# Kernel tuning notes

Measured on AMD Instinct MI355X. Metric: run time of the kernel, lower is better.

## Reference

```python
import jax, jax.numpy as jnp
import numpy as np

N_NODES = 100000
N_EDGES = 500000
N_REL = 3
IN_F, HID_F, OUT_F = 128, 128, 128
H_HALF = OUT_F // 2  # BiLSTM hidden per direction


def setup_inputs() -> dict:
    key = jax.random.key(0)
    ks = jax.random.split(key, 16)
    s = 0.05
    inp = {
        "x": jax.random.normal(ks[0], (N_NODES, IN_F), jnp.float32),
        "src": jax.random.randint(ks[1], (N_REL, N_EDGES), 0, N_NODES),
        "dst": jax.random.randint(ks[2], (N_REL, N_EDGES), 0, N_NODES),
        # per-relation GraphConv weights (layer 1 and 2)
        "W1": jax.random.normal(ks[3], (N_REL, IN_F, HID_F), jnp.float32) * s,
        "b1": jnp.zeros((N_REL, HID_F), jnp.float32),
        "W2": jax.random.normal(ks[4], (N_REL, HID_F, OUT_F), jnp.float32) * s,
        "b2": jnp.zeros((N_REL, OUT_F), jnp.float32),
        # BiLSTM (1 layer, seq_len=1); PyTorch gate order i,f,g,o
        "Wih_f": jax.random.normal(ks[5], (4 * H_HALF, OUT_F), jnp.float32) * s,
        "Whh_f": jax.random.normal(ks[6], (4 * H_HALF, H_HALF), jnp.float32) * s,
        "bih_f": jnp.zeros((4 * H_HALF,), jnp.float32),
        "bhh_f": jnp.zeros((4 * H_HALF,), jnp.float32),
        "Wih_b": jax.random.normal(ks[7], (4 * H_HALF, OUT_F), jnp.float32) * s,
        "Whh_b": jax.random.normal(ks[8], (4 * H_HALF, H_HALF), jnp.float32) * s,
        "bih_b": jnp.zeros((4 * H_HALF,), jnp.float32),
        "bhh_b": jnp.zeros((4 * H_HALF,), jnp.float32),
    }
    return inp


def _hetero_conv(x, src, dst, W, b):
    """HeteroGraphConv(GraphConv, norm='both'), mean-aggregated over relations.
    x: [N,Din]; src,dst: [R,E]; W: [R,Din,Dout]; b: [R,Dout] -> [N,Dout]."""
    n = x.shape[0]

    def rel_conv(s, d, w, bb):
        ones = jnp.ones(s.shape[0], x.dtype)
        deg_out = jnp.clip(jax.ops.segment_sum(ones, s, num_segments=n), 1.0)
        deg_in = jnp.clip(jax.ops.segment_sum(ones, d, num_segments=n), 1.0)
        # weight first (in_feats >= out_feats path in DGL); math-equivalent
        xw = (x * jax.lax.rsqrt(deg_out)[:, None]) @ w          # [N,Dout]
        agg = jax.ops.segment_sum(xw[s], d, num_segments=n)     # [N,Dout]
        return agg * jax.lax.rsqrt(deg_in)[:, None] + bb

    outs = jax.vmap(rel_conv)(src, dst, W, b)  # [R,N,Dout]
    return jnp.mean(outs, axis=0)


def _lstm_step(x, Wih, bih, bhh):
    # single LSTM step from zero (h0, c0); Whh contributes nothing
    g = x @ Wih.T + bih + bhh
    i, f, gg, o = jnp.split(g, 4, axis=-1)
    c = jax.nn.sigmoid(i) * jnp.tanh(gg)
    return jax.nn.sigmoid(o) * jnp.tanh(c)


def reference(x, src, dst, W1, b1, W2, b2,
              Wih_f, Whh_f, bih_f, bhh_f,
              Wih_b, Whh_b, bih_b, bhh_b):
    h = jax.nn.relu(_hetero_conv(x, src, dst, W1, b1))
    h = _hetero_conv(h, src, dst, W2, b2)          # [N, OUT_F]
    hf = _lstm_step(h, Wih_f, bih_f, bhh_f)        # [N, H_HALF]
    hb = _lstm_step(h, Wih_b, bih_b, bhh_b)        # [N, H_HALF]
    return jnp.concatenate([hf, hb], axis=-1)      # [N, OUT_F]
```

## Files before the change

kernel.cpp:

```cpp
#include <hip/hip_runtime.h>
#include <hip/hip_fp16.h>
#include <math.h>

#define NN 100000
#define NE 500000
#define NREL 3
#define F 128
#define SCAN_BLK 1024
#define NBLK ((NN + SCAN_BLK - 1) / SCAN_BLK)
#define CH 25000
#define NCH 4

#define RANGE 16384
#define NRANGE 7
#define NPAD (NRANGE * RANGE)
#define EC 20
#define EPC (NE / EC)

typedef __attribute__((ext_vector_type(8))) short bf16x8;
typedef __attribute__((ext_vector_type(4))) float f32x4;

__device__ __forceinline__ float sigm(float x) { return 1.f / (1.f + __expf(-x)); }

__device__ __forceinline__ unsigned bf16rne(float x) {
  unsigned u = __float_as_uint(x);
  return (u + 0x7FFFu + ((u >> 16) & 1u)) >> 16;
}
__device__ __forceinline__ void split1(float x, unsigned& h, unsigned& l) {
  h = bf16rne(x);
  float hf = __uint_as_float(h << 16);
  l = bf16rne(x - hf);
}

__global__ __launch_bounds__(256) void hist_part(const int* __restrict__ src,
                                                 const int* __restrict__ dst,
                                                 int* __restrict__ part) {
  int x = blockIdx.x & 7, q = blockIdx.x >> 3;
  int g = q % NRANGE;
  int rc2 = x + 8 * (q / NRANGE);
  int a = rc2 / (NREL * EC);
  int rcl = rc2 % (NREL * EC);
  int r = rcl / EC, c = rcl % EC;
  __shared__ int h[RANGE];
  for (int i = threadIdx.x; i < RANGE; i += 256) h[i] = 0;
  __syncthreads();
  const int* idx = (a ? dst : src) + (size_t)r * NE + (size_t)c * EPC;
  const int4* v4 = (const int4*)idx;
  int lo = g * RANGE;
  for (int i = threadIdx.x; i < EPC / 4; i += 256) {
    int4 v = v4[i];
    int t;
    t = v.x - lo; if ((unsigned)t < RANGE) atomicAdd(&h[t], 1);
    t = v.y - lo; if ((unsigned)t < RANGE) atomicAdd(&h[t], 1);
    t = v.z - lo; if ((unsigned)t < RANGE) atomicAdd(&h[t], 1);
    t = v.w - lo; if ((unsigned)t < RANGE) atomicAdd(&h[t], 1);
  }
  __syncthreads();
  int* op = part + (((size_t)a * NREL + r) * EC + c) * NPAD + (size_t)g * RANGE;
  for (int i = threadIdx.x; i < RANGE; i += 256) op[i] = h[i];
}

__global__ void reduce_part(const int* __restrict__ part, int* __restrict__ cnt_out,
                            int* __restrict__ cnt_in) {
  int i = blockIdx.x * blockDim.x + threadIdx.x;
  if (i >= 2 * NREL * NN) return;
  int a = i / (NREL * NN);
  int rn = i - a * (NREL * NN);
  const int* p = part + ((size_t)a * NREL + rn / NN) * EC * NPAD + (rn % NN);
  int s = 0;
#pragma unroll
  for (int c = 0; c < EC; ++c) s += p[(size_t)c * NPAD];
  (a ? cnt_in : cnt_out)[rn] = s;
}

__global__ void make_rs(const int* __restrict__ cnt_out, const int* __restrict__ cnt_in,
                        float* __restrict__ rs_out, float* __restrict__ rs_in3) {
  int i = blockIdx.x * blockDim.x + threadIdx.x;
  if (i >= NREL * NN) return;
  int c0 = cnt_out[i];
  rs_out[i] = rsqrtf((float)(c0 < 1 ? 1 : c0));
  int c1 = cnt_in[i];
  rs_in3[i] = rsqrtf((float)(c1 < 1 ? 1 : c1)) * (1.f / 3.f);
}

__global__ __launch_bounds__(256) void scan1(const int* __restrict__ cnt,
                                             int* __restrict__ excl, int* __restrict__ bsums) {
  int rb = blockIdx.x;
  int r = rb / NBLK, blk = rb % NBLK;
  int tid = (int)threadIdx.x;
  int v[4]; int sum = 0;
#pragma unroll
  for (int i = 0; i < 4; ++i) {
    int idx = blk * SCAN_BLK + tid * 4 + i;
    int c = (idx < NN) ? cnt[r * NN + idx] : 0;
    v[i] = sum; sum += c;
  }
  __shared__ int ts[256];
  ts[tid] = sum;
  __syncthreads();
  for (int off = 1; off < 256; off <<= 1) {
    int t = (tid >= off) ? ts[tid - off] : 0;
    __syncthreads();
    ts[tid] += t;
    __syncthreads();
  }
  int texcl = tid ? ts[tid - 1] : 0;
#pragma unroll
  for (int i = 0; i < 4; ++i) {
    int idx = blk * SCAN_BLK + tid * 4 + i;
    if (idx < NN) excl[r * NN + idx] = texcl + v[i];
  }
  if (tid == 255) bsums[rb] = ts[255];
}

__global__ __launch_bounds__(128) void scan2(int* __restrict__ bsums) {
  int r = blockIdx.x;
  int tid = (int)threadIdx.x;
  __shared__ int ts[128];
  ts[tid] = (tid < NBLK) ? bsums[r * NBLK + tid] : 0;
  __syncthreads();
  for (int off = 1; off < 128; off <<= 1) {
    int t = (tid >= off) ? ts[tid - off] : 0;
    __syncthreads();
    ts[tid] += t;
    __syncthreads();
  }
  if (tid < NBLK) bsums[r * NBLK + tid] = tid ? ts[tid - 1] : 0;
}

__global__ void scan3(int* __restrict__ row_ptr, const int* __restrict__ bsums) {
  int i = blockIdx.x * blockDim.x + threadIdx.x;
  if (i >= NREL * NN) return;
  int r = i / NN, idx = i - r * NN, blk = idx / SCAN_BLK;
  row_ptr[i] += bsums[r * NBLK + blk];
}

__global__ void chunk_prefix(int* __restrict__ part_dst, const int* __restrict__ row_ptr) {
  int i = blockIdx.x * blockDim.x + threadIdx.x;
  if (i >= NREL * NN) return;
  int r = i / NN, node = i - r * NN;
  int* p = part_dst + (size_t)r * EC * NPAD + node;
  int run = row_ptr[i];
#pragma unroll
  for (int c = 0; c < EC; ++c) {
    int t = p[(size_t)c * NPAD];
    p[(size_t)c * NPAD] = run;
    run += t;
  }
}

__global__ void make_pay(const int* __restrict__ src, const float* __restrict__ rs_out,
                         int2* __restrict__ pay) {
  int i = blockIdx.x * blockDim.x + threadIdx.x;
  if (i >= NREL * NE) return;
  int r = i / NE;
  int s = src[i];
  pay[i] = make_int2(s, __float_as_int(rs_out[r * NN + s]));
}

__global__ __launch_bounds__(256) void place_part(const int* __restrict__ dst,
                                                  const int2* __restrict__ pay,
                                                  const int* __restrict__ part_dst,
                                                  int2* __restrict__ ses) {
  int x = blockIdx.x & 7, q = blockIdx.x >> 3;
  int g = q % NRANGE;
  int rc = x + 8 * (q / NRANGE);
  if (rc >= NREL * EC) return;
  int r = rc / EC, c = rc % EC;
  __shared__ int cur[RANGE];
  const int* pc = part_dst + ((size_t)r * EC + c) * NPAD + (size_t)g * RANGE;
  for (int i = threadIdx.x; i < RANGE; i += 256) cur[i] = pc[i];
  __syncthreads();
  int lo = g * RANGE;
  const int4* d4 = (const int4*)(dst + (size_t)r * NE + (size_t)c * EPC);
  const int4* p4 = (const int4*)(pay + (size_t)r * NE + (size_t)c * EPC);
  int2* sesr = ses + (size_t)r * NE;
  for (int i = threadIdx.x; i < EPC / 4; i += 256) {
    int4 dv = d4[i];
    int4 pa = p4[2 * i], pb = p4[2 * i + 1];
    int t;
    t = dv.x - lo; if ((unsigned)t < RANGE) { int pos = atomicAdd(&cur[t], 1); sesr[pos] = make_int2(pa.x, pa.y); }
    t = dv.y - lo; if ((unsigned)t < RANGE) { int pos = atomicAdd(&cur[t], 1); sesr[pos] = make_int2(pa.z, pa.w); }
    t = dv.z - lo; if ((unsigned)t < RANGE) { int pos = atomicAdd(&cur[t], 1); sesr[pos] = make_int2(pb.x, pb.y); }
    t = dv.w - lo; if ((unsigned)t < RANGE) { int pos = atomicAdd(&cur[t], 1); sesr[pos] = make_int2(pb.z, pb.w); }
  }
}

__global__ void prep_small(const float* __restrict__ b1, const float* __restrict__ b2,
                           const float* __restrict__ bif, const float* __restrict__ bhf,
                           const float* __restrict__ bib, const float* __restrict__ bhb,
                           float* __restrict__ bbar1, float* __restrict__ bbar2,
                           float* __restrict__ bselw) {
  int t = (int)threadIdx.x;
  if (t < 128) {
    bbar1[t] = (b1[t] + b1[128 + t] + b1[256 + t]) * (1.f / 3.f);
  } else if (t < 256) {
    int j = t - 128;
    bbar2[j] = (b2[j] + b2[128 + j] + b2[256 + j]) * (1.f / 3.f);
  } else if (t < 640) {
    int m = t - 256;
    int g = m >> 7, j = m & 127, dir = j >> 6, jj = j & 63;
    int grow = (g == 0) ? jj : (g == 1) ? (128 + jj) : (192 + jj);
    bselw[m] = dir ? (bib[grow] + bhb[grow]) : (bif[grow] + bhf[grow]);
  }
}

__global__ void wt_split(const float* __restrict__ W, ushort* __restrict__ th,
                         ushort* __restrict__ tl) {
  int i = blockIdx.x * blockDim.x + threadIdx.x;
  if (i >= 128 * 384) return;
  int n = i / 384, k = i % 384;
  float v = W[(size_t)k * 128 + n];
  unsigned h, l; split1(v, h, l);
  th[i] = (ushort)h; tl[i] = (ushort)l;
}

__global__ void pack_w_split(const float* __restrict__ Wf, const float* __restrict__ Wb,
                             ushort* __restrict__ ph, ushort* __restrict__ pl) {
  int i = blockIdx.x * blockDim.x + threadIdx.x;
  if (i >= 384 * 128) return;
  int m = i / 128, k = i % 128;
  int g = m >> 7, j = m & 127, dir = j >> 6, jj = j & 63;
  int grow = (g == 0) ? jj : (g == 1) ? (128 + jj) : (192 + jj);
  float v = (dir ? Wb : Wf)[(size_t)grow * 128 + k];
  unsigned h, l; split1(v, h, l);
  ph[i] = (ushort)h; pl[i] = (ushort)l;
}

__global__ void cvt_f16(const float* __restrict__ in, ushort* __restrict__ o16) {
  int i = blockIdx.x * blockDim.x + threadIdx.x;
  if (i >= NN * (F / 4)) return;
  float4 v = ((const float4*)in)[i];
  __half2 a = __floats2half2_rn(v.x, v.y);
  __half2 b = __floats2half2_rn(v.z, v.w);
  ((uint2*)o16)[i] = make_uint2(*(unsigned*)&a, *(unsigned*)&b);
}

__global__ __launch_bounds__(256) void gather3(
    const ushort* __restrict__ table, const int2* __restrict__ ses,
    const int* __restrict__ row_ptr, const int* __restrict__ cnt,
    const float* __restrict__ rs_in3, ushort* __restrict__ z_h,
    ushort* __restrict__ z_l, int n0) {
  int wid = (int)threadIdx.x >> 6, lane = (int)threadIdx.x & 63;
  int gw = blockIdx.x * 4 + wid;
  int r = gw / CH;
  int n = n0 + (gw - r * CH);
  int base = r * NN + n;
  int beg = row_ptr[base], c = cnt[base];
  const int2* el = ses + (size_t)r * NE + beg;
  int half = lane >> 5, cl = lane & 31;
  const uint2* x2 = (const uint2*)table + cl;
  float4 acc = make_float4(0.f, 0.f, 0.f, 0.f);

  int p = 0;
  while (p < c) {
    int rem = c - p; if (rem > 16) rem = 16;
    int2 es = make_int2(0, 0);
    if (lane < rem) es = el[p + lane];
    uint2 rw[8]; float scv[8];
#pragma unroll
    for (int j = 0; j < 8; ++j) {
      int e = 2 * j + half;
      int idx = (e < rem) ? e : 0;
      int s = __shfl(es.x, idx);
      float sc = __int_as_float(__shfl(es.y, idx));
      if (e >= rem) sc = 0.f;
      if (2 * j < rem) {
        rw[j] = x2[(size_t)s * 32];
        scv[j] = sc;
      }
    }
#pragma unroll
    for (int j = 0; j < 8; ++j) {
      if (2 * j < rem) {
        float2 f0 = __half22float2(*(__half2*)&rw[j].x);
        float2 f1 = __half22float2(*(__half2*)&rw[j].y);
        float sc = scv[j];
        acc.x = fmaf(f0.x, sc, acc.x); acc.y = fmaf(f0.y, sc, acc.y);
        acc.z = fmaf(f1.x, sc, acc.z); acc.w = fmaf(f1.y, sc, acc.w);
      }
    }
    p += rem;
  }

  acc.x += __shfl_xor(acc.x, 32);
  acc.y += __shfl_xor(acc.y, 32);
  acc.z += __shfl_xor(acc.z, 32);
  acc.w += __shfl_xor(acc.w, 32);
  float ci = rs_in3[base];
  unsigned h[4], l[4];
  split1(acc.x * ci, h[0], l[0]); split1(acc.y * ci, h[1], l[1]);
  split1(acc.z * ci, h[2], l[2]); split1(acc.w * ci, h[3], l[3]);
  size_t zo = (size_t)(n - n0) * 384 + r * 128 + cl * 4;
  if (half == 0) {
    *(ushort2*)(z_h + zo) = make_ushort2((ushort)h[0], (ushort)h[1]);
    *(ushort2*)(z_h + zo + 2) = make_ushort2((ushort)h[2], (ushort)h[3]);
  } else {
    *(ushort2*)(z_l + zo) = make_ushort2((ushort)l[0], (ushort)l[1]);
    *(ushort2*)(z_l + zo + 2) = make_ushort2((ushort)l[2], (ushort)l[3]);
  }
}

__device__ __forceinline__ int swz(int row, int slot) {
  return row * 32 + ((slot ^ ((row >> 1) & 3)) << 3);
}

template <bool RELU, bool OUT16>
__global__ __launch_bounds__(256) void gemm_mfma(
    const ushort* __restrict__ zh, const ushort* __restrict__ zl,
    const ushort* __restrict__ wth, const ushort* __restrict__ wtl,
    const float* __restrict__ bias, void* __restrict__ Hout, int n0) {
  __shared__ ushort Ash[64 * 32], Asl[64 * 32], Bsh[128 * 32], Bsl[128 * 32];
  const int row0 = blockIdx.x * 64;
  const int t = (int)threadIdx.x;
  const int wn = t >> 6, l = t & 63, lr = l & 15, lk = l >> 4;
  f32x4 acc[4][2];
#pragma unroll
  for (int a = 0; a < 4; ++a)
#pragma unroll
    for (int b = 0; b < 2; ++b) acc[a][b] = (f32x4){0.f, 0.f, 0.f, 0.f};

  for (int kt = 0; kt < 12; ++kt) {
    __syncthreads();
    {
      int rr = t >> 2, slot = t & 3;
      size_t go = (size_t)(row0 + rr) * 384 + kt * 32 + slot * 8;
      uint4 vh = make_uint4(0, 0, 0, 0), vl = make_uint4(0, 0, 0, 0);
      if (row0 + rr < CH) { vh = *(const uint4*)(zh + go); vl = *(const uint4*)(zl + go); }
      *(uint4*)&Ash[swz(rr, slot)] = vh;
      *(uint4*)&Asl[swz(rr, slot)] = vl;
    }
#pragma unroll
    for (int i = 0; i < 2; ++i) {
      int s = i * 256 + t;
      int nn_ = s >> 2, slot = s & 3;
      size_t go = (size_t)nn_ * 384 + kt * 32 + slot * 8;
      *(uint4*)&Bsh[swz(nn_, slot)] = *(const uint4*)(wth + go);
      *(uint4*)&Bsl[swz(nn_, slot)] = *(const uint4*)(wtl + go);
    }
    __syncthreads();
    bf16x8 ah[4], al[4], bh[2], bl[2];
#pragma unroll
    for (int mf = 0; mf < 4; ++mf) {
      int row = mf * 16 + lr;
      int off = swz(row, lk);
      ah[mf] = *(const bf16x8*)&Ash[off];
      al[mf] = *(const bf16x8*)&Asl[off];
    }
#pragma unroll
    for (int f = 0; f < 2; ++f) {
      int col = wn * 32 + f * 16 + lr;
      int off = swz(col, lk);
      bh[f] = *(const bf16x8*)&Bsh[off];
      bl[f] = *(const bf16x8*)&Bsl[off];
    }
#pragma unroll
    for (int mf = 0; mf < 4; ++mf)
#pragma unroll
      for (int f = 0; f < 2; ++f) {
        acc[mf][f] = __builtin_amdgcn_mfma_f32_16x16x32_bf16(ah[mf], bh[f], acc[mf][f], 0, 0, 0);
        acc[mf][f] = __builtin_amdgcn_mfma_f32_16x16x32_bf16(ah[mf], bl[f], acc[mf][f], 0, 0, 0);
        acc[mf][f] = __builtin_amdgcn_mfma_f32_16x16x32_bf16(al[mf], bh[f], acc[mf][f], 0, 0, 0);
      }
  }
#pragma unroll
  for (int mf = 0; mf < 4; ++mf)
#pragma unroll
    for (int f = 0; f < 2; ++f) {
      int col = wn * 32 + f * 16 + lr;
      float bv = bias[col];
#pragma unroll
      for (int reg = 0; reg < 4; ++reg) {
        int row = row0 + mf * 16 + lk * 4 + reg;
        if (row < CH) {
          float v = acc[mf][f][reg] + bv;
          if (RELU) v = fmaxf(v, 0.f);
          if (OUT16) {
            __half hv = __float2half_rn(v);
            ((ushort*)Hout)[(size_t)(n0 + row) * 128 + col] = *(ushort*)&hv;
          } else {
            ((float*)Hout)[(size_t)(n0 + row) * 128 + col] = v;
          }
        }
      }
    }
}

__global__ __launch_bounds__(512) void lstm_mfma(
    const float* __restrict__ H, const ushort* __restrict__ wph,
    const ushort* __restrict__ wpl, const float* __restrict__ bselw,
    float* __restrict__ out) {
  __shared__ ushort Ash[128 * 32], Asl[128 * 32], Bsh[384 * 32], Bsl[384 * 32];
  const int row0 = blockIdx.x * 128;
  const int t = (int)threadIdx.x;
  const int wid = t >> 6, wm = wid >> 2, wn = wid & 3;
  const int l = t & 63, lr = l & 15, lk = l >> 4;

  int j0 = wn * 16 + lr, j1 = (wn + 4) * 16 + lr;
  float bi0 = bselw[j0], bg0 = bselw[128 + j0], bo0 = bselw[256 + j0];
  float bi1 = bselw[j1], bg1 = bselw[128 + j1], bo1 = bselw[256 + j1];

  f32x4 acc[4][6];
#pragma unroll
  for (int a = 0; a < 4; ++a)
#pragma unroll
    for (int b = 0; b < 6; ++b) acc[a][b] = (f32x4){0.f, 0.f, 0.f, 0.f};

  for (int kt = 0; kt < 4; ++kt) {
    __syncthreads();
    {
      int rr = t >> 2, slot = t & 3;
      int grow = row0 + rr;
      float v[8];
      if (grow < NN) {
        float4 a0 = *(const float4*)(H + (size_t)grow * 128 + kt * 32 + slot * 8);
        float4 a1 = *(const float4*)(H + (size_t)grow * 128 + kt * 32 + slot * 8 + 4);
        v[0] = a0.x; v[1] = a0.y; v[2] = a0.z; v[3] = a0.w;
        v[4] = a1.x; v[5] = a1.y; v[6] = a1.z; v[7] = a1.w;
      } else {
#pragma unroll
        for (int q = 0; q < 8; ++q) v[q] = 0.f;
      }
      unsigned h[8], lo[8];
#pragma unroll
      for (int q = 0; q < 8; ++q) split1(v[q], h[q], lo[q]);
      uint4 hv = make_uint4(h[0] | (h[1] << 16), h[2] | (h[3] << 16),
                            h[4] | (h[5] << 16), h[6] | (h[7] << 16));
      uint4 lv = make_uint4(lo[0] | (lo[1] << 16), lo[2] | (lo[3] << 16),
                            lo[4] | (lo[5] << 16), lo[6] | (lo[7] << 16));
      *(uint4*)&Ash[swz(rr, slot)] = hv;
      *(uint4*)&Asl[swz(rr, slot)] = lv;
    }
#pragma unroll
    for (int i = 0; i < 3; ++i) {
      int s = i * 512 + t;
      int nn_ = s >> 2, slot = s & 3;
      size_t go = (size_t)nn_ * 128 + kt * 32 + slot * 8;
      *(uint4*)&Bsh[swz(nn_, slot)] = *(const uint4*)(wph + go);
      *(uint4*)&Bsl[swz(nn_, slot)] = *(const uint4*)(wpl + go);
    }
    __syncthreads();
    bf16x8 ah[4], al[4];
#pragma unroll
    for (int mf = 0; mf < 4; ++mf) {
      int row = wm * 64 + mf * 16 + lr;
      int off = swz(row, lk);
      ah[mf] = *(const bf16x8*)&Ash[off];
      al[mf] = *(const bf16x8*)&Asl[off];
    }
#pragma unroll
    for (int tt = 0; tt < 6; ++tt) {
      int col = (wn + 4 * tt) * 16 + lr;
      int off = swz(col, lk);
      bf16x8 bh = *(const bf16x8*)&Bsh[off];
      bf16x8 bl = *(const bf16x8*)&Bsl[off];
#pragma unroll
      for (int mf = 0; mf < 4; ++mf) {
        acc[mf][tt] = __builtin_amdgcn_mfma_f32_16x16x32_bf16(ah[mf], bh, acc[mf][tt], 0, 0, 0);
        acc[mf][tt] = __builtin_amdgcn_mfma_f32_16x16x32_bf16(ah[mf], bl, acc[mf][tt], 0, 0, 0);
        acc[mf][tt] = __builtin_amdgcn_mfma_f32_16x16x32_bf16(al[mf], bh, acc[mf][tt], 0, 0, 0);
      }
    }
  }
#pragma unroll
  for (int mf = 0; mf < 4; ++mf)
#pragma unroll
    for (int reg = 0; reg < 4; ++reg) {
      int row = row0 + wm * 64 + mf * 16 + lk * 4 + reg;
      if (row < NN) {
        float iv0 = acc[mf][0][reg] + bi0, gv0 = acc[mf][2][reg] + bg0, ov0 = acc[mf][4][reg] + bo0;
        float cc0 = sigm(iv0) * tanhf(gv0);
        out[(size_t)row * 128 + j0] = sigm(ov0) * tanhf(cc0);
        float iv1 = acc[mf][1][reg] + bi1, gv1 = acc[mf][3][reg] + bg1, ov1 = acc[mf][5][reg] + bo1;
        float cc1 = sigm(iv1) * tanhf(gv1);
        out[(size_t)row * 128 + j1] = sigm(ov1) * tanhf(cc1);
      }
    }
}

extern "C" void kernel_launch(void* const* d_in, const int* in_sizes, int n_in,
                              void* d_out, int out_size, void* d_ws, size_t ws_size,
                              hipStream_t stream) {
  const float* x = (const float*)d_in[0];
  const int* src = (const int*)d_in[1];
  const int* dst = (const int*)d_in[2];
  const float* W1 = (const float*)d_in[3];
  const float* b1 = (const float*)d_in[4];
  const float* W2 = (const float*)d_in[5];
  const float* b2 = (const float*)d_in[6];
  const float* Wih_f = (const float*)d_in[7];
  const float* bih_f = (const float*)d_in[9];
  const float* bhh_f = (const float*)d_in[10];
  const float* Wih_b = (const float*)d_in[11];
  const float* bih_b = (const float*)d_in[13];
  const float* bhh_b = (const float*)d_in[14];
  float* out = (float*)d_out;

  char* wp = (char*)d_ws;
  float* rs_out = (float*)wp;          wp += (size_t)3 * NN * 4;
  float* rs_in3 = (float*)wp;          wp += (size_t)3 * NN * 4;
  int* cnt_out = (int*)wp;             wp += (size_t)3 * NN * 4;
  int* cnt_in = (int*)wp;              wp += (size_t)3 * NN * 4;
  int* row_ptr = (int*)wp;             wp += (size_t)3 * NN * 4;
  int* bsums = (int*)wp;               wp += 4096;
  int2* ses = (int2*)wp;               wp += (size_t)3 * NE * 8;
  ushort* wt1h = (ushort*)wp;          wp += (size_t)128 * 384 * 2;
  ushort* wt1l = (ushort*)wp;          wp += (size_t)128 * 384 * 2;
  ushort* wt2h = (ushort*)wp;          wp += (size_t)128 * 384 * 2;
  ushort* wt2l = (ushort*)wp;          wp += (size_t)128 * 384 * 2;
  ushort* wph = (ushort*)wp;           wp += (size_t)384 * 128 * 2;
  ushort* wpl = (ushort*)wp;           wp += (size_t)384 * 128 * 2;
  float* bbar1 = (float*)wp;           wp += 512;
  float* bbar2 = (float*)wp;           wp += 512;
  float* bselw = (float*)wp;           wp += 2048;
  ushort* z_h = (ushort*)wp;           wp += (size_t)CH * 384 * 2;
  ushort* z_l = (ushort*)wp;           wp += (size_t)CH * 384 * 2;
  ushort* x16 = (ushort*)wp;           wp += (size_t)NN * F * 2;
  ushort* h116 = (ushort*)wp;          wp += (size_t)NN * F * 2;

  int* part = (int*)z_h;
  int* part_dst = part + (size_t)NREL * EC * NPAD;
  int2* pay = (int2*)h116;

  hist_part<<<8 * ((2 * NREL * EC + 7) / 8) * NRANGE, 256, 0, stream>>>(src, dst, part);
  reduce_part<<<(2 * NREL * NN + 255) / 256, 256, 0, stream>>>(part, cnt_out, cnt_in);
  make_rs<<<(NREL * NN + 255) / 256, 256, 0, stream>>>(cnt_out, cnt_in, rs_out, rs_in3);
  scan1<<<NREL * NBLK, 256, 0, stream>>>(cnt_in, row_ptr, bsums);
  scan2<<<NREL, 128, 0, stream>>>(bsums);
  scan3<<<(NREL * NN + 255) / 256, 256, 0, stream>>>(row_ptr, bsums);
  chunk_prefix<<<(NREL * NN + 255) / 256, 256, 0, stream>>>(part_dst, row_ptr);
  make_pay<<<(NREL * NE + 255) / 256, 256, 0, stream>>>(src, rs_out, pay);
  place_part<<<8 * ((NREL * EC + 7) / 8) * NRANGE, 256, 0, stream>>>(dst, pay, part_dst, ses);

  prep_small<<<1, 640, 0, stream>>>(b1, b2, bih_f, bhh_f, bih_b, bhh_b, bbar1, bbar2, bselw);
  wt_split<<<192, 256, 0, stream>>>(W1, wt1h, wt1l);
  wt_split<<<192, 256, 0, stream>>>(W2, wt2h, wt2l);
  pack_w_split<<<192, 256, 0, stream>>>(Wih_f, Wih_b, wph, wpl);
  cvt_f16<<<(NN * 32 + 255) / 256, 256, 0, stream>>>(x, x16);

  for (int c = 0; c < NCH; ++c) {
    gather3<<<3 * CH / 4, 256, 0, stream>>>(x16, ses, row_ptr, cnt_in, rs_in3, z_h, z_l, c * CH);
    gemm_mfma<true, true><<<(CH + 63) / 64, 256, 0, stream>>>(z_h, z_l, wt1h, wt1l, bbar1, h116, c * CH);
  }
  for (int c = 0; c < NCH; ++c) {
    gather3<<<3 * CH / 4, 256, 0, stream>>>(h116, ses, row_ptr, cnt_in, rs_in3, z_h, z_l, c * CH);
    gemm_mfma<false, false><<<(CH + 63) / 64, 256, 0, stream>>>(z_h, z_l, wt2h, wt2l, bbar2, out, c * CH);
  }
  lstm_mfma<<<(NN + 127) / 128, 512, 0, stream>>>(out, wph, wpl, bselw, out);
}
```

Measured before the change: 570.3 us.

## Store gathered activations as fp16 and fuse layer-2 GEMM with LSTM

The gather kernel now writes one fp16 intermediate instead of separate bf16 hi/lo planes, and the GEMM kernels split it into hi/lo bf16 when staging into shared memory. The layer-2 GraphConv GEMM is fused with the LSTM projection, so the layer-2 output stays in LDS and is never written to and re-read from global memory as fp32. This cuts intermediate memory traffic and one kernel launch. In exchange it adds fp16 rounding of the aggregated features and uses a larger LDS footprint and 512-thread blocks, which may lower occupancy.

```diff
diff --git a/kernel.cpp b/kernel.cpp
--- a/kernel.cpp
+++ b/kernel.cpp
@@ -30,6 +30,10 @@
   h = bf16rne(x);
   float hf = __uint_as_float(h << 16);
   l = bf16rne(x - hf);
+}
+
+__device__ __forceinline__ int swz(int row, int slot) {
+  return row * 32 + ((slot ^ ((row >> 1) & 3)) << 3);
 }
 
 __global__ __launch_bounds__(256) void hist_part(const int* __restrict__ src,
@@ -239,8 +243,7 @@
 __global__ __launch_bounds__(256) void gather3(
     const ushort* __restrict__ table, const int2* __restrict__ ses,
     const int* __restrict__ row_ptr, const int* __restrict__ cnt,
-    const float* __restrict__ rs_in3, ushort* __restrict__ z_h,
-    ushort* __restrict__ z_l, int n0) {
+    const float* __restrict__ rs_in3, ushort* __restrict__ z16, int n0) {
   int wid = (int)threadIdx.x >> 6, lane = (int)threadIdx.x & 63;
   int gw = blockIdx.x * 4 + wid;
   int r = gw / CH;
@@ -287,29 +290,34 @@
   acc.y += __shfl_xor(acc.y, 32);
   acc.z += __shfl_xor(acc.z, 32);
   acc.w += __shfl_xor(acc.w, 32);
-  float ci = rs_in3[base];
-  unsigned h[4], l[4];
-  split1(acc.x * ci, h[0], l[0]); split1(acc.y * ci, h[1], l[1]);
-  split1(acc.z * ci, h[2], l[2]); split1(acc.w * ci, h[3], l[3]);
-  size_t zo = (size_t)(n - n0) * 384 + r * 128 + cl * 4;
   if (half == 0) {
-    *(ushort2*)(z_h + zo) = make_ushort2((ushort)h[0], (ushort)h[1]);
-    *(ushort2*)(z_h + zo + 2) = make_ushort2((ushort)h[2], (ushort)h[3]);
-  } else {
-    *(ushort2*)(z_l + zo) = make_ushort2((ushort)l[0], (ushort)l[1]);
-    *(ushort2*)(z_l + zo + 2) = make_ushort2((ushort)l[2], (ushort)l[3]);
-  }
-}
-
-__device__ __forceinline__ int swz(int row, int slot) {
-  return row * 32 + ((slot ^ ((row >> 1) & 3)) << 3);
-}
-
-template <bool RELU, bool OUT16>
-__global__ __launch_bounds__(256) void gemm_mfma(
-    const ushort* __restrict__ zh, const ushort* __restrict__ zl,
+    float ci = rs_in3[base];
+    __half2 p0 = __floats2half2_rn(acc.x * ci, acc.y * ci);
+    __half2 p1 = __floats2half2_rn(acc.z * ci, acc.w * ci);
+    size_t zo = (size_t)(n - n0) * 384 + r * 128 + cl * 4;
+    *(uint2*)(z16 + zo) = make_uint2(*(unsigned*)&p0, *(unsigned*)&p1);
+  }
+}
+
+__device__ __forceinline__ void cvt_split8(uint4 v, uint4& hv, uint4& lv) {
+  float f[8];
+  *(float2*)&f[0] = __half22float2(*(__half2*)&v.x);
+  *(float2*)&f[2] = __half22float2(*(__half2*)&v.y);
+  *(float2*)&f[4] = __half22float2(*(__half2*)&v.z);
+  *(float2*)&f[6] = __half22float2(*(__half2*)&v.w);
+  unsigned h[8], l[8];
+#pragma unroll
+  for (int q = 0; q < 8; ++q) split1(f[q], h[q], l[q]);
+  hv = make_uint4(h[0] | (h[1] << 16), h[2] | (h[3] << 16),
+                  h[4] | (h[5] << 16), h[6] | (h[7] << 16));
+  lv = make_uint4(l[0] | (l[1] << 16), l[2] | (l[3] << 16),
+                  l[4] | (l[5] << 16), l[6] | (l[7] << 16));
+}
+
+__global__ __launch_bounds__(256) void gemm_mfma1(
+    const ushort* __restrict__ z16,
     const ushort* __restrict__ wth, const ushort* __restrict__ wtl,
-    const float* __restrict__ bias, void* __restrict__ Hout, int n0) {
+    const float* __restrict__ bias, ushort* __restrict__ Hout, int n0) {
   __shared__ ushort Ash[64 * 32], Asl[64 * 32], Bsh[128 * 32], Bsl[128 * 32];
   const int row0 = blockIdx.x * 64;
   const int t = (int)threadIdx.x;
@@ -324,11 +332,12 @@
     __syncthreads();
     {
       int rr = t >> 2, slot = t & 3;
-      size_t go = (size_t)(row0 + rr) * 384 + kt * 32 + slot * 8;
-      uint4 vh = make_uint4(0, 0, 0, 0), vl = make_uint4(0, 0, 0, 0);
-      if (row0 + rr < CH) { vh = *(const uint4*)(zh + go); vl = *(const uint4*)(zl + go); }
-      *(uint4*)&Ash[swz(rr, slot)] = vh;
-      *(uint4*)&Asl[swz(rr, slot)] = vl;
+      uint4 v = make_uint4(0, 0, 0, 0);
+      if (row0 + rr < CH)
+        v = *(const uint4*)(z16 + (size_t)(row0 + rr) * 384 + kt * 32 + slot * 8);
+      uint4 hv, lv; cvt_split8(v, hv, lv);
+      *(uint4*)&Ash[swz(rr, slot)] = hv;
+      *(uint4*)&Asl[swz(rr, slot)] = lv;
     }
 #pragma unroll
     for (int i = 0; i < 2; ++i) {
@@ -342,15 +351,13 @@
     bf16x8 ah[4], al[4], bh[2], bl[2];
 #pragma unroll
     for (int mf = 0; mf < 4; ++mf) {
-      int row = mf * 16 + lr;
-      int off = swz(row, lk);
+      int off = swz(mf * 16 + lr, lk);
       ah[mf] = *(const bf16x8*)&Ash[off];
       al[mf] = *(const bf16x8*)&Asl[off];
     }
 #pragma unroll
     for (int f = 0; f < 2; ++f) {
-      int col = wn * 32 + f * 16 + lr;
-      int off = swz(col, lk);
+      int off = swz(wn * 32 + f * 16 + lr, lk);
       bh[f] = *(const bf16x8*)&Bsh[off];
       bl[f] = *(const bf16x8*)&Bsl[off];
     }
@@ -373,107 +380,154 @@
       for (int reg = 0; reg < 4; ++reg) {
         int row = row0 + mf * 16 + lk * 4 + reg;
         if (row < CH) {
-          float v = acc[mf][f][reg] + bv;
-          if (RELU) v = fmaxf(v, 0.f);
-          if (OUT16) {
-            __half hv = __float2half_rn(v);
-            ((ushort*)Hout)[(size_t)(n0 + row) * 128 + col] = *(ushort*)&hv;
-          } else {
-            ((float*)Hout)[(size_t)(n0 + row) * 128 + col] = v;
-          }
+          float v = fmaxf(acc[mf][f][reg] + bv, 0.f);
+          __half hv = __float2half_rn(v);
+          Hout[(size_t)(n0 + row) * 128 + col] = *(ushort*)&hv;
         }
       }
     }
 }
 
-__global__ __launch_bounds__(512) void lstm_mfma(
-    const float* __restrict__ H, const ushort* __restrict__ wph,
-    const ushort* __restrict__ wpl, const float* __restrict__ bselw,
-    float* __restrict__ out) {
-  __shared__ ushort Ash[128 * 32], Asl[128 * 32], Bsh[384 * 32], Bsl[384 * 32];
-  const int row0 = blockIdx.x * 128;
+__global__ __launch_bounds__(512) void gemm2_lstm(
+    const ushort* __restrict__ z16,
+    const ushort* __restrict__ wth, const ushort* __restrict__ wtl,
+    const ushort* __restrict__ wph, const ushort* __restrict__ wpl,
+    const float* __restrict__ bbar2, const float* __restrict__ bselw,
+    float* __restrict__ out, int n0) {
+  __shared__ ushort lds[40960];
+  ushort* A1h = lds;
+  ushort* A1l = lds + 2048;
+  ushort* B1h = lds + 4096;
+  ushort* B1l = lds + 8192;
+  ushort* A2h = lds;
+  ushort* A2l = lds + 8192;
+  ushort* B3h = lds + 16384;
+  ushort* B3l = lds + 28672;
+
+  const int row0 = blockIdx.x * 64;
   const int t = (int)threadIdx.x;
-  const int wid = t >> 6, wm = wid >> 2, wn = wid & 3;
-  const int l = t & 63, lr = l & 15, lk = l >> 4;
-
-  int j0 = wn * 16 + lr, j1 = (wn + 4) * 16 + lr;
+  const int wid = t >> 6, l = t & 63, lr = l & 15, lk = l >> 4;
+
+  f32x4 acc1[4];
+#pragma unroll
+  for (int a = 0; a < 4; ++a) acc1[a] = (f32x4){0.f, 0.f, 0.f, 0.f};
+
+  for (int kt = 0; kt < 12; ++kt) {
+    __syncthreads();
+    if (t < 256) {
+      int rr = t >> 2, slot = t & 3;
+      uint4 v = make_uint4(0, 0, 0, 0);
+      if (row0 + rr < CH)
+        v = *(const uint4*)(z16 + (size_t)(row0 + rr) * 384 + kt * 32 + slot * 8);
+      uint4 hv, lv; cvt_split8(v, hv, lv);
+      *(uint4*)&A1h[swz(rr, slot)] = hv;
+      *(uint4*)&A1l[swz(rr, slot)] = lv;
+    }
+    {
+      int nn_ = t >> 2, slot = t & 3;
+      size_t go = (size_t)nn_ * 384 + kt * 32 + slot * 8;
+      *(uint4*)&B1h[swz(nn_, slot)] = *(const uint4*)(wth + go);
+      *(uint4*)&B1l[swz(nn_, slot)] = *(const uint4*)(wtl + go);
+    }
+    __syncthreads();
+    bf16x8 ah[4], al[4];
+#pragma unroll
+    for (int mf = 0; mf < 4; ++mf) {
+      int off = swz(mf * 16 + lr, lk);
+      ah[mf] = *(const bf16x8*)&A1h[off];
+      al[mf] = *(const bf16x8*)&A1l[off];
+    }
+    int offb = swz(wid * 16 + lr, lk);
+    bf16x8 bh = *(const bf16x8*)&B1h[offb];
+    bf16x8 bl = *(const bf16x8*)&B1l[offb];
+#pragma unroll
+    for (int mf = 0; mf < 4; ++mf) {
+      acc1[mf] = __builtin_amdgcn_mfma_f32_16x16x32_bf16(ah[mf], bh, acc1[mf], 0, 0, 0);
+      acc1[mf] = __builtin_amdgcn_mfma_f32_16x16x32_bf16(ah[mf], bl, acc1[mf], 0, 0, 0);
+      acc1[mf] = __builtin_amdgcn_mfma_f32_16x16x32_bf16(al[mf], bh, acc1[mf], 0, 0, 0);
+    }
+  }
+
+  __syncthreads();
+  {
+    int colc = wid * 16 + lr;
+    float bb = bbar2[colc];
+#pragma unroll
+    for (int mf = 0; mf < 4; ++mf)
+#pragma unroll
+      for (int reg = 0; reg < 4; ++reg) {
+        int rowc = mf * 16 + lk * 4 + reg;
+        float v = acc1[mf][reg] + bb;
+        unsigned h, lo2; split1(v, h, lo2);
+        int sl2 = (colc >> 3) ^ (rowc & 7);
+        int addr = rowc * 128 + (sl2 << 3) + (colc & 7);
+        A2h[addr] = (ushort)h;
+        A2l[addr] = (ushort)lo2;
+      }
+  }
+  __syncthreads();
+
+  const int wm = wid >> 2, wn3 = wid & 3;
+  f32x4 acc3[2][6];
+#pragma unroll
+  for (int a = 0; a < 2; ++a)
+#pragma unroll
+    for (int b = 0; b < 6; ++b) acc3[a][b] = (f32x4){0.f, 0.f, 0.f, 0.f};
+
+  for (int kt = 0; kt < 4; ++kt) {
+    if (kt) __syncthreads();
+#pragma unroll
+    for (int i = 0; i < 3; ++i) {
+      int s = i * 512 + t;
+      int m = s >> 2, slot = s & 3;
+      size_t go = (size_t)m * 128 + kt * 32 + slot * 8;
+      *(uint4*)&B3h[swz(m, slot)] = *(const uint4*)(wph + go);
+      *(uint4*)&B3l[swz(m, slot)] = *(const uint4*)(wpl + go);
+    }
+    __syncthreads();
+    bf16x8 ah2[2], al2[2];
+#pragma unroll
+    for (int mf = 0; mf < 2; ++mf) {
+      int row = wm * 32 + mf * 16 + lr;
+      int kslot = kt * 4 + lk;
+      int sl2 = kslot ^ (row & 7);
+      int addr = row * 128 + (sl2 << 3);
+      ah2[mf] = *(const bf16x8*)&A2h[addr];
+      al2[mf] = *(const bf16x8*)&A2l[addr];
+    }
+#pragma unroll
+    for (int tt = 0; tt < 6; ++tt) {
+      int m = (wn3 + 4 * tt) * 16 + lr;
+      int off = swz(m, lk);
+      bf16x8 bh = *(const bf16x8*)&B3h[off];
+      bf16x8 bl = *(const bf16x8*)&B3l[off];
+#pragma unroll
+      for (int mf = 0; mf < 2; ++mf) {
+        acc3[mf][tt] = __builtin_amdgcn_mfma_f32_16x16x32_bf16(ah2[mf], bh, acc3[mf][tt], 0, 0, 0);
+        acc3[mf][tt] = __builtin_amdgcn_mfma_f32_16x16x32_bf16(ah2[mf], bl, acc3[mf][tt], 0, 0, 0);
+        acc3[mf][tt] = __builtin_amdgcn_mfma_f32_16x16x32_bf16(al2[mf], bh, acc3[mf][tt], 0, 0, 0);
+      }
+    }
+  }
+
+  int j0 = wn3 * 16 + lr, j1 = j0 + 64;
   float bi0 = bselw[j0], bg0 = bselw[128 + j0], bo0 = bselw[256 + j0];
   float bi1 = bselw[j1], bg1 = bselw[128 + j1], bo1 = bselw[256 + j1];
-
-  f32x4 acc[4][6];
-#pragma unroll
-  for (int a = 0; a < 4; ++a)
-#pragma unroll
-    for (int b = 0; b < 6; ++b) acc[a][b] = (f32x4){0.f, 0.f, 0.f, 0.f};
-
-  for (int kt = 0; kt < 4; ++kt) {
-    __syncthreads();
-    {
-      int rr = t >> 2, slot = t & 3;
-      int grow = row0 + rr;
-      float v[8];
-      if (grow < NN) {
-        float4 a0 = *(const float4*)(H + (size_t)grow * 128 + kt * 32 + slot * 8);
-        float4 a1 = *(const float4*)(H + (size_t)grow * 128 + kt * 32 + slot * 8 + 4);
-        v[0] = a0.x; v[1] = a0.y; v[2] = a0.z; v[3] = a0.w;
-        v[4] = a1.x; v[5] = a1.y; v[6] = a1.z; v[7] = a1.w;
-      } else {
-#pragma unroll
-        for (int q = 0; q < 8; ++q) v[q] = 0.f;
-      }
-      unsigned h[8], lo[8];
-#pragma unroll
-      for (int q = 0; q < 8; ++q) split1(v[q], h[q], lo[q]);
-      uint4 hv = make_uint4(h[0] | (h[1] << 16), h[2] | (h[3] << 16),
-                            h[4] | (h[5] << 16), h[6] | (h[7] << 16));
-      uint4 lv = make_uint4(lo[0] | (lo[1] << 16), lo[2] | (lo[3] << 16),
-                            lo[4] | (lo[5] << 16), lo[6] | (lo[7] << 16));
-      *(uint4*)&Ash[swz(rr, slot)] = hv;
-      *(uint4*)&Asl[swz(rr, slot)] = lv;
-    }
-#pragma unroll
-    for (int i = 0; i < 3; ++i) {
-      int s = i * 512 + t;
-      int nn_ = s >> 2, slot = s & 3;
-      size_t go = (size_t)nn_ * 128 + kt * 32 + slot * 8;
-      *(uint4*)&Bsh[swz(nn_, slot)] = *(const uint4*)(wph + go);
-      *(uint4*)&Bsl[swz(nn_, slot)] = *(const uint4*)(wpl + go);
-    }
-    __syncthreads();
-    bf16x8 ah[4], al[4];
-#pragma unroll
-    for (int mf = 0; mf < 4; ++mf) {
-      int row = wm * 64 + mf * 16 + lr;
-      int off = swz(row, lk);
-      ah[mf] = *(const bf16x8*)&Ash[off];
-      al[mf] = *(const bf16x8*)&Asl[off];
-    }
-#pragma unroll
-    for (int tt = 0; tt < 6; ++tt) {
-      int col = (wn + 4 * tt) * 16 + lr;
-      int off = swz(col, lk);
-      bf16x8 bh = *(const bf16x8*)&Bsh[off];
-      bf16x8 bl = *(const bf16x8*)&Bsl[off];
-#pragma unroll
-      for (int mf = 0; mf < 4; ++mf) {
-        acc[mf][tt] = __builtin_amdgcn_mfma_f32_16x16x32_bf16(ah[mf], bh, acc[mf][tt], 0, 0, 0);
-        acc[mf][tt] = __builtin_amdgcn_mfma_f32_16x16x32_bf16(ah[mf], bl, acc[mf][tt], 0, 0, 0);
-        acc[mf][tt] = __builtin_amdgcn_mfma_f32_16x16x32_bf16(al[mf], bh, acc[mf][tt], 0, 0, 0);
-      }
-    }
-  }
-#pragma unroll
-  for (int mf = 0; mf < 4; ++mf)
+#pragma unroll
+  for (int mf = 0; mf < 2; ++mf)
 #pragma unroll
     for (int reg = 0; reg < 4; ++reg) {
-      int row = row0 + wm * 64 + mf * 16 + lk * 4 + reg;
-      if (row < NN) {
-        float iv0 = acc[mf][0][reg] + bi0, gv0 = acc[mf][2][reg] + bg0, ov0 = acc[mf][4][reg] + bo0;
-        float cc0 = sigm(iv0) * tanhf(gv0);
-        out[(size_t)row * 128 + j0] = sigm(ov0) * tanhf(cc0);
-        float iv1 = acc[mf][1][reg] + bi1, gv1 = acc[mf][3][reg] + bg1, ov1 = acc[mf][5][reg] + bo1;
-        float cc1 = sigm(iv1) * tanhf(gv1);
-        out[(size_t)row * 128 + j1] = sigm(ov1) * tanhf(cc1);
+      int grow = wm * 32 + mf * 16 + lk * 4 + reg;
+      if (row0 + grow < CH) {
+        size_t orow = (size_t)(n0 + row0 + grow) * 128;
+        float iv0 = acc3[mf][0][reg] + bi0, gv0 = acc3[mf][2][reg] + bg0,
+              ov0 = acc3[mf][4][reg] + bo0;
+        float c0 = sigm(iv0) * tanhf(gv0);
+        out[orow + j0] = sigm(ov0) * tanhf(c0);
+        float iv1 = acc3[mf][1][reg] + bi1, gv1 = acc3[mf][3][reg] + bg1,
+              ov1 = acc3[mf][5][reg] + bo1;
+        float c1 = sigm(iv1) * tanhf(gv1);
+        out[orow + j1] = sigm(ov1) * tanhf(c1);
       }
     }
 }
@@ -513,16 +567,15 @@
   float* bbar1 = (float*)wp;           wp += 512;
   float* bbar2 = (float*)wp;           wp += 512;
   float* bselw = (float*)wp;           wp += 2048;
-  ushort* z_h = (ushort*)wp;           wp += (size_t)CH * 384 * 2;
-  ushort* z_l = (ushort*)wp;           wp += (size_t)CH * 384 * 2;
+  ushort* z16 = (ushort*)wp;           wp += (size_t)CH * 384 * 2;
   ushort* x16 = (ushort*)wp;           wp += (size_t)NN * F * 2;
   ushort* h116 = (ushort*)wp;          wp += (size_t)NN * F * 2;
 
-  int* part = (int*)z_h;
+  int* part = (int*)z16;
   int* part_dst = part + (size_t)NREL * EC * NPAD;
-  int2* pay = (int2*)h116;
-
-  hist_part<<<8 * ((2 * NREL * EC + 7) / 8) * NRANGE, 256, 0, stream>>>(src, dst, part);
+  int2* pay = (int2*)((char*)h116 + ((size_t)12 << 20));
+
+  hist_part<<<2 * NREL * EC * NRANGE, 256, 0, stream>>>(src, dst, part);
   reduce_part<<<(2 * NREL * NN + 255) / 256, 256, 0, stream>>>(part, cnt_out, cnt_in);
   make_rs<<<(NREL * NN + 255) / 256, 256, 0, stream>>>(cnt_out, cnt_in, rs_out, rs_in3);
   scan1<<<NREL * NBLK, 256, 0, stream>>>(cnt_in, row_ptr, bsums);
@@ -539,12 +592,12 @@
   cvt_f16<<<(NN * 32 + 255) / 256, 256, 0, stream>>>(x, x16);
 
   for (int c = 0; c < NCH; ++c) {
-    gather3<<<3 * CH / 4, 256, 0, stream>>>(x16, ses, row_ptr, cnt_in, rs_in3, z_h, z_l, c * CH);
-    gemm_mfma<true, true><<<(CH + 63) / 64, 256, 0, stream>>>(z_h, z_l, wt1h, wt1l, bbar1, h116, c * CH);
+    gather3<<<3 * CH / 4, 256, 0, stream>>>(x16, ses, row_ptr, cnt_in, rs_in3, z16, c * CH);
+    gemm_mfma1<<<(CH + 63) / 64, 256, 0, stream>>>(z16, wt1h, wt1l, bbar1, h116, c * CH);
   }
   for (int c = 0; c < NCH; ++c) {
-    gather3<<<3 * CH / 4, 256, 0, stream>>>(h116, ses, row_ptr, cnt_in, rs_in3, z_h, z_l, c * CH);
-    gemm_mfma<false, false><<<(CH + 63) / 64, 256, 0, stream>>>(z_h, z_l, wt2h, wt2l, bbar2, out, c * CH);
-  }
-  lstm_mfma<<<(NN + 127) / 128, 512, 0, stream>>>(out, wph, wpl, bselw, out);
-}
+    gather3<<<3 * CH / 4, 256, 0, stream>>>(h116, ses, row_ptr, cnt_in, rs_in3, z16, c * CH);
+    gemm2_lstm<<<(CH + 63) / 64, 512, 0, stream>>>(z16, wt2h, wt2l, wph, wpl,
+                                                   bbar2, bselw, out, c * CH);
+  }
+}
```

Measured after the change: 520.0 us. -8.8%, faster.
